# Kernel optimization log

Hardware: AMD Instinct MI355X
Metric: run time of the kernel (lower is better)

Reference implementation:

```python
import jax, jax.numpy as jnp
import numpy as np
import math

B, S, D, H, MAX_LEN = 4, 1024, 1024, 16, 1024
DH = D // H  # 64

def setup_inputs() -> dict:
    key = jax.random.key(0)
    ks = jax.random.split(key, 9)
    s = 1.0 / math.sqrt(D)
    return {
        "q":  jax.random.normal(ks[0], (B, S, D), jnp.float32),
        "kv": jax.random.normal(ks[1], (B, S, D), jnp.float32),
        "Wq": jax.random.normal(ks[2], (D, D), jnp.float32) * s,
        "bq": jax.random.normal(ks[3], (D,), jnp.float32) * s,
        "Wk": jax.random.normal(ks[4], (D, D), jnp.float32) * s,
        "bk": jax.random.normal(ks[5], (D,), jnp.float32) * s,
        "Wv": jax.random.normal(ks[6], (D, D), jnp.float32) * s,
        "bv": jax.random.normal(ks[7], (D,), jnp.float32) * s,
        "Er": jax.random.normal(ks[8], (MAX_LEN, DH), jnp.float32),
    }

def _skew(QEr):
    # QEr: [B, H, S, S]. Music-Transformer skew trick:
    # pad one zero column on the left, reshape, drop first row.
    b, h, r, c = QEr.shape
    padded = jnp.pad(QEr, ((0, 0), (0, 0), (0, 0), (1, 0)))  # [b,h,r,c+1]
    reshaped = padded.reshape(b, h, c + 1, r)
    return reshaped[:, :, 1:, :]  # [b,h,r,c]

def reference(q, kv, Wq, bq, Wk, bk, Wv, bv, Er):
    b, s, d = kv.shape
    # projections (nn.Linear: x @ W + b with W stored [in,out])
    k = (kv @ Wk + bk).reshape(b, s, H, DH).transpose(0, 2, 3, 1)  # [b,h,dh,s]
    v = (kv @ Wv + bv).reshape(b, s, H, DH).transpose(0, 2, 1, 3)  # [b,h,s,dh]
    qh = (q @ Wq + bq).reshape(b, s, H, DH).transpose(0, 2, 1, 3)  # [b,h,s,dh]
    # relative position scores
    Er_t = Er[MAX_LEN - s:, :].T            # [dh, s]
    QEr = jnp.einsum('bhsd,dt->bhst', qh, Er_t)
    Srel = _skew(QEr)                        # [b,h,s,s]
    # content scores
    QK = jnp.einsum('bhsd,bhdt->bhst', qh, k)
    attn = (QK + Srel) / math.sqrt(DH)
    causal = jnp.tril(jnp.ones((s, s), dtype=bool))[None, None]
    attn = jnp.where(causal, attn, -jnp.inf)
    attn = jax.nn.softmax(attn, axis=-1)
    out = jnp.einsum('bhst,bhtd->bhsd', attn, v)
    out = out.transpose(0, 2, 1, 3).reshape(b, s, d)
    return out  # dropout is identity (p=0 / eval)
```

## Files before the change

kernel.cpp:

```cpp
#include <hip/hip_runtime.h>
#include <hip/hip_bf16.h>

typedef __bf16 bf16x8 __attribute__((ext_vector_type(8)));
typedef __bf16 bf16x4 __attribute__((ext_vector_type(4)));
typedef float  f32x4  __attribute__((ext_vector_type(4)));
typedef unsigned __attribute__((may_alias)) u32a;

#define MFMA_B16(a, b, c) __builtin_amdgcn_mfma_f32_16x16x32_bf16((a), (b), (c), 0, 0, 0)

static constexpr int Bk  = 4;
static constexpr int Sk  = 1024;
static constexpr int Dk  = 1024;
static constexpr int Hk  = 16;
static constexpr int DHk = 64;

static constexpr size_t QH_OFF = 0;
static constexpr size_t K_OFF  = 4194304;
static constexpr size_t VT_OFF = 8388608;
static constexpr size_t WT_OFF = 12582912;
static constexpr size_t ER_OFF = 15728640;
static constexpr size_t WS_ELEMS = 15794176;

__device__ __forceinline__ void load_lds16(const void* g, void* l) {
    __builtin_amdgcn_global_load_lds((const __attribute__((address_space(1))) void*)g,
                                     (__attribute__((address_space(3))) void*)l, 16, 0, 0);
}

template<int CTRL>
__device__ __forceinline__ float dppf(float x) {
    int v = __builtin_bit_cast(int, x);
    return __builtin_bit_cast(float,
        __builtin_amdgcn_update_dpp(v, v, CTRL, 0xF, 0xF, false));
}
__device__ __forceinline__ float rmax16(float x) {
    x = fmaxf(x, dppf<0x128>(x));
    x = fmaxf(x, dppf<0x124>(x));
    x = fmaxf(x, dppf<0x122>(x));
    x = fmaxf(x, dppf<0x121>(x));
    return x;
}
__device__ __forceinline__ float rsum16(float x) {
    x += dppf<0x128>(x);
    x += dppf<0x124>(x);
    x += dppf<0x122>(x);
    x += dppf<0x121>(x);
    return x;
}
__device__ __forceinline__ unsigned pk_bf16(float lo, float hi) {
    unsigned r;
    asm("v_cvt_pk_bf16_f32 %0, %1, %2" : "=v"(r) : "v"(lo), "v"(hi));
    return r;
}

__global__ void prep_kernel(const float* __restrict__ Wq, const float* __restrict__ Wk,
                            const float* __restrict__ Wv, const float* __restrict__ Er,
                            __bf16* __restrict__ wt, __bf16* __restrict__ erb)
{
    __shared__ float tile[64][65];
    const int z = blockIdx.z;
    const int tid = threadIdx.x;
    if (z == 3) {
        int idx = (blockIdx.y * 16 + blockIdx.x) * 256 + tid;
        erb[idx] = (__bf16)Er[idx];
        return;
    }
    const float* W = (z == 0) ? Wq : (z == 1 ? Wk : Wv);
    __bf16* dst = wt + (size_t)z * Dk * Dk;
    const int k0 = blockIdx.y * 64, n0 = blockIdx.x * 64;
    #pragma unroll
    for (int j = 0; j < 16; ++j) {
        int idx = tid + j * 256; int r = idx >> 6, c = idx & 63;
        tile[r][c] = W[(size_t)(k0 + r) * Dk + n0 + c];
    }
    __syncthreads();
    #pragma unroll
    for (int j = 0; j < 16; ++j) {
        int idx = tid + j * 256; int r = idx >> 6, c = idx & 63;
        dst[(size_t)(n0 + r) * Dk + k0 + c] = (__bf16)tile[c][r];
    }
}

__global__ __launch_bounds__(256) void proj_kernel(
    const float* __restrict__ Xq, const float* __restrict__ Xkv,
    const float* __restrict__ bq, const float* __restrict__ bk,
    const float* __restrict__ bv, const __bf16* __restrict__ wt,
    __bf16* __restrict__ qh, __bf16* __restrict__ kws, __bf16* __restrict__ vt)
{
    __shared__ __align__(16) float  Al[128 * 32];
    __shared__ __align__(16) __bf16 Bl[128 * 32];

    const int z = blockIdx.z;
    const float* X    = (z == 0) ? Xq : Xkv;
    const float* bias = (z == 0) ? bq : (z == 1 ? bk : bv);
    const __bf16* Wz  = wt + (size_t)z * Dk * Dk;

    const int m0   = blockIdx.x * 128;
    const int n0   = blockIdx.y * 128;
    const int tid  = threadIdx.x;
    const int lane = tid & 63;
    const int w    = tid >> 6;
    const int wr   = w >> 1, wc = w & 1;
    const int l15  = lane & 15;
    const int g    = lane >> 4;

    const float* asrc[4];
    int adst[4];
    #pragma unroll
    for (int i = 0; i < 4; ++i) {
        const int c = w * 4 + i;
        asrc[i] = X + (size_t)(m0 + c * 8 + (lane >> 3)) * Dk + (((lane & 7) ^ (lane >> 3)) << 2);
        adst[i] = c * 1024 + lane * 16;
    }
    const __bf16* bsrc[2];
    int bdst[2];
    #pragma unroll
    for (int i = 0; i < 2; ++i) {
        const int c = w * 2 + i;
        bsrc[i] = Wz + (size_t)(n0 + c * 16 + (lane >> 2)) * Dk + (((lane & 3) ^ ((lane >> 3) & 3)) << 3);
        bdst[i] = c * 1024 + lane * 16;
    }

    int aoff0[4], aoff1[4], boff[4];
    #pragma unroll
    for (int m = 0; m < 4; ++m) {
        const int row = wr * 64 + m * 16 + l15;
        aoff0[m] = row * 128 + (((2 * g)     ^ (l15 & 7)) << 4);
        aoff1[m] = row * 128 + (((2 * g + 1) ^ (l15 & 7)) << 4);
    }
    #pragma unroll
    for (int n = 0; n < 4; ++n) {
        const int row = wc * 64 + n * 16 + l15;
        boff[n] = row * 64 + ((g ^ ((l15 >> 1) & 3)) << 4);
    }

    const f32x4 fz = {0.f, 0.f, 0.f, 0.f};
    f32x4 acc[4][4];
    #pragma unroll
    for (int m = 0; m < 4; ++m)
        #pragma unroll
        for (int n = 0; n < 4; ++n) acc[m][n] = fz;

    const char* Alc = (const char*)Al;
    const char* Blc = (const char*)Bl;

    for (int ks = 0; ks < Dk / 32; ++ks) {
        #pragma unroll
        for (int i = 0; i < 4; ++i)
            load_lds16(asrc[i], (char*)Al + adst[i]);
        #pragma unroll
        for (int i = 0; i < 2; ++i)
            load_lds16(bsrc[i], (char*)Bl + bdst[i]);
        #pragma unroll
        for (int i = 0; i < 4; ++i) asrc[i] += 32;
        #pragma unroll
        for (int i = 0; i < 2; ++i) bsrc[i] += 32;
        __syncthreads();

        bf16x8 bf[4];
        #pragma unroll
        for (int n = 0; n < 4; ++n)
            bf[n] = *(const bf16x8*)(Blc + boff[n]);
        bf16x8 af[4];
        #pragma unroll
        for (int m = 0; m < 4; ++m) {
            f32x4 x0 = *(const f32x4*)(Alc + aoff0[m]);
            f32x4 x1 = *(const f32x4*)(Alc + aoff1[m]);
            bf16x8 a;
            a[0] = (__bf16)x0[0]; a[1] = (__bf16)x0[1]; a[2] = (__bf16)x0[2]; a[3] = (__bf16)x0[3];
            a[4] = (__bf16)x1[0]; a[5] = (__bf16)x1[1]; a[6] = (__bf16)x1[2]; a[7] = (__bf16)x1[3];
            af[m] = a;
        }

        #pragma unroll
        for (int m = 0; m < 4; ++m)
            #pragma unroll
            for (int n = 0; n < 4; ++n)
                acc[m][n] = MFMA_B16(af[m], bf[n], acc[m][n]);
        __syncthreads();
    }

    #pragma unroll
    for (int n = 0; n < 4; ++n) {
        const float bb = bias[n0 + wc * 64 + n * 16 + l15];
        #pragma unroll
        for (int m = 0; m < 4; ++m)
            #pragma unroll
            for (int r = 0; r < 4; ++r) acc[m][n][r] += bb;
    }

    const int b   = m0 >> 10;
    const int s0t = (m0 & 1023) + wr * 64;
    const int h   = (n0 + wc * 64) >> 6;

    if (z < 2) {
        __bf16* dst = (z == 0) ? qh : kws;
        const size_t rowbase = (size_t)(b * Hk + h) * Sk;
        #pragma unroll
        for (int m = 0; m < 4; ++m) {
            #pragma unroll
            for (int r = 0; r < 4; ++r) {
                const int s = s0t + m * 16 + g * 4 + r;
                __bf16* drow = dst + (rowbase + s) * DHk;
                #pragma unroll
                for (int n = 0; n < 4; ++n)
                    drow[n * 16 + l15] = (__bf16)acc[m][n][r];
            }
        }
    } else {
        const size_t hb = (size_t)(b * Hk + h) * DHk;
        #pragma unroll
        for (int m = 0; m < 4; ++m) {
            const int sb = s0t + m * 16 + g * 4;
            #pragma unroll
            for (int n = 0; n < 4; ++n) {
                const int dh = n * 16 + l15;
                bf16x4 pk;
                #pragma unroll
                for (int r = 0; r < 4; ++r) pk[r] = (__bf16)acc[m][n][r];
                *(bf16x4*)(vt + (hb + dh) * Sk + sb) = pk;
            }
        }
    }
}

__device__ __forceinline__ void front_tile(
    const char* Kc, const __bf16* __restrict__ erb, int jb, int l15, int g,
    const bf16x8 (&aq)[2], f32x4 (&sc)[4], f32x4 (&gf)[5])
{
    const f32x4 fz = {0.f, 0.f, 0.f, 0.f};
    #pragma unroll
    for (int j = 0; j < 4; ++j) sc[j] = fz;
    #pragma unroll
    for (int jj = 0; jj < 5; ++jj) gf[jj] = fz;
    #pragma unroll
    for (int kt = 0; kt < 2; ++kt) {
        bf16x8 kb[4];
        #pragma unroll
        for (int j = 0; j < 4; ++j)
            kb[j] = *(const bf16x8*)(Kc + (j * 16 + l15) * 128 + ((((kt << 2) | g) ^ (l15 & 7)) << 4));
        __builtin_amdgcn_s_setprio(1);
        #pragma unroll
        for (int j = 0; j < 4; ++j)
            sc[j] = MFMA_B16(aq[kt], kb[j], sc[j]);
        __builtin_amdgcn_s_setprio(0);
    }
    #pragma unroll
    for (int kt = 0; kt < 2; ++kt) {
        bf16x8 ec[5];
        #pragma unroll
        for (int jj = 0; jj < 5; ++jj) {
            int jr = jb + jj * 16 + l15;
            jr = (jr > 1023) ? 1023 : jr;
            ec[jj] = *(const bf16x8*)(erb + (size_t)jr * DHk + kt * 32 + g * 8);
        }
        __builtin_amdgcn_s_setprio(1);
        #pragma unroll
        for (int jj = 0; jj < 5; ++jj)
            gf[jj] = MFMA_B16(aq[kt], ec[jj], gf[jj]);
        __builtin_amdgcn_s_setprio(0);
    }
}

__global__ __launch_bounds__(256, 3) void attn_kernel(
    const __bf16* __restrict__ qh, const __bf16* __restrict__ kws,
    const __bf16* __restrict__ vt, const __bf16* __restrict__ erb,
    float* __restrict__ out)
{
    __shared__ __align__(16) __bf16 Kl[2][4096];
    __shared__ __align__(16) __bf16 Vl[3][4096];
    __shared__ __align__(16) __bf16 P_lds[4][16][64];

    const int tid  = threadIdx.x;
    const int lane = tid & 63;
    const int w    = tid >> 6;
    const int l15  = lane & 15;
    const int g    = lane >> 4;

    const int lid   = blockIdx.x;
    const int bh    = lid & 63;
    const int strip = 15 - (lid >> 6);
    const int ntw   = strip + 1;
    const int sw    = strip * 64 + w * 16;

    const __bf16* kbase = kws + (size_t)bh * Sk * DHk;
    const __bf16* vbase = vt  + (size_t)bh * DHk * Sk;
    const __bf16* qbase = qh  + ((size_t)bh * Sk + sw) * DHk;

    __bf16 (*Pw)[64] = P_lds[w];

    const int trow   = tid >> 3;
    const int tslot  = tid & 7;
    const int srcoff = (tslot ^ (trow & 7)) << 3;
    char* kd0 = (char*)Kl + tid * 16;
    char* vd0 = (char*)Vl + tid * 16;

    bf16x8 aq[2];
    aq[0] = *(const bf16x8*)(qbase + l15 * DHk + g * 8);
    aq[1] = *(const bf16x8*)(qbase + l15 * DHk + 32 + g * 8);

    const f32x4 fz = {0.f, 0.f, 0.f, 0.f};
    f32x4 O[4];
    float m_[4], l_[4];
    #pragma unroll
    for (int n = 0; n < 4; ++n) O[n] = fz;
    #pragma unroll
    for (int r = 0; r < 4; ++r) { m_[r] = -1e30f; l_[r] = 0.f; }

    const float SCL = 0.125f * 1.44269504088896f;

    load_lds16(kbase + (size_t)trow * DHk + srcoff,        kd0);
    load_lds16(kbase + (size_t)(32 + trow) * DHk + srcoff, kd0 + 4096);
    load_lds16(vbase + (size_t)trow * Sk + srcoff,         vd0);
    load_lds16(vbase + (size_t)(32 + trow) * Sk + srcoff,  vd0 + 4096);
    __builtin_amdgcn_sched_barrier(0);
    asm volatile("s_waitcnt vmcnt(0)" ::: "memory");
    __builtin_amdgcn_sched_barrier(0);
    __builtin_amdgcn_s_barrier();
    __builtin_amdgcn_sched_barrier(0);

    f32x4 scA[4], scB[4], gf[5];
    front_tile((const char*)Kl, erb, 1008 - sw, l15, g, aq, scA, gf);

    int vcur = 0, vnxt = 1;

    for (int it = 0; it < ntw; ++it) {
        const int t0  = it * 64;
        const int cur = it & 1;
        const bool more = (it + 1 < ntw);

        if (more) {
            const int t0n = t0 + 64;
            char* kd = kd0 + (cur ^ 1) * 8192;
            char* vd = (char*)Vl + vnxt * 8192 + tid * 16;
            load_lds16(kbase + (size_t)(t0n + trow) * DHk + srcoff,      kd);
            load_lds16(kbase + (size_t)(t0n + 32 + trow) * DHk + srcoff, kd + 4096);
            load_lds16(vbase + (size_t)trow * Sk + t0n + srcoff,         vd);
            load_lds16(vbase + (size_t)(32 + trow) * Sk + t0n + srcoff,  vd + 4096);
        }
        __builtin_amdgcn_sched_barrier(0);
        asm volatile("s_waitcnt vmcnt(0)" ::: "memory");
        __builtin_amdgcn_sched_barrier(0);
        __builtin_amdgcn_s_barrier();
        __builtin_amdgcn_sched_barrier(0);

        #pragma unroll
        for (int r = 0; r < 4; ++r) {
            const int rr  = g * 4 + r;
            const int sft = 15 - rr;
            const int src = (g << 4) + ((l15 + sft) & 15);
            const bool hi = (l15 + sft) >= 16;
            float h[5];
            #pragma unroll
            for (int jj = 0; jj < 5; ++jj) h[jj] = __shfl(gf[jj][r], src);
            const int s = sw + rr;
            #pragma unroll
            for (int j = 0; j < 4; ++j) {
                float gval = hi ? h[j + 1] : h[j];
                float v = (scA[j][r] + gval) * SCL;
                int t = t0 + j * 16 + l15;
                scA[j][r] = (t > s) ? -1e30f : v;
            }
        }

        if (more)
            front_tile((const char*)Kl + (cur ^ 1) * 8192, erb,
                       t0 + 64 - sw + 1008, l15, g, aq, scB, gf);

        float mt[4];
        #pragma unroll
        for (int r = 0; r < 4; ++r)
            mt[r] = rmax16(fmaxf(fmaxf(scA[0][r], scA[1][r]), fmaxf(scA[2][r], scA[3][r])));

        bool grow = (mt[0] > m_[0] + 8.f) || (mt[1] > m_[1] + 8.f) ||
                    (mt[2] > m_[2] + 8.f) || (mt[3] > m_[3] + 8.f);
        if (__any(grow)) {
            #pragma unroll
            for (int r = 0; r < 4; ++r) {
                float mnew = fmaxf(m_[r], mt[r]);
                float scl  = exp2f(m_[r] - mnew);
                l_[r] *= scl;
                m_[r]  = mnew;
                #pragma unroll
                for (int n = 0; n < 4; ++n) O[n][r] *= scl;
            }
        }
        #pragma unroll
        for (int r = 0; r < 4; ++r) {
            float rs = 0.f;
            #pragma unroll
            for (int j = 0; j < 4; ++j) {
                float p = exp2f(scA[j][r] - m_[r]);
                scA[j][r] = p; rs += p;
            }
            l_[r] += rsum16(rs);
        }

        {
            const int p01 = l15 & 1;
            #pragma unroll
            for (int j = 0; j < 4; ++j) {
                const int slot = 2 * j + (l15 >> 3);
                #pragma unroll
                for (int h2 = 0; h2 < 2; ++h2) {
                    float a0 = scA[j][h2];
                    float a2 = scA[j][h2 + 2];
                    float b0 = dppf<0xB1>(a0);
                    float b2 = dppf<0xB1>(a2);
                    float lo = p01 ? b2 : a0;
                    float hi = p01 ? a2 : b0;
                    unsigned wd = pk_bf16(lo, hi);
                    const int row = g * 4 + h2 + (p01 ? 2 : 0);
                    const int byteoff = row * 128 + (((slot ^ (row & 7)) << 4) | ((l15 & 6) << 1));
                    *(u32a*)((char*)Pw + byteoff) = wd;
                }
            }
        }
        asm volatile("" ::: "memory");
        __builtin_amdgcn_sched_barrier(0);

        const char* Vc = (const char*)Vl + vcur * 8192;
        __builtin_amdgcn_s_setprio(1);
        #pragma unroll
        for (int kt = 0; kt < 2; ++kt) {
            bf16x8 pa = *(const bf16x8*)((const char*)Pw + l15 * 128 +
                                         ((((kt << 2) | g) ^ (l15 & 7)) << 4));
            #pragma unroll
            for (int n = 0; n < 4; ++n) {
                bf16x8 vbf = *(const bf16x8*)(Vc + (n * 16 + l15) * 128 + ((((kt << 2) | g) ^ (l15 & 7)) << 4));
                O[n] = MFMA_B16(pa, vbf, O[n]);
            }
        }
        __builtin_amdgcn_s_setprio(0);

        if (more) {
            #pragma unroll
            for (int j = 0; j < 4; ++j) scA[j] = scB[j];
        }
        vcur = vnxt;
        vnxt = (vnxt == 2) ? 0 : vnxt + 1;
    }

    const int b = bh >> 4, h = bh & 15;
    float* obase = out + ((size_t)b * Sk + sw) * Dk + h * DHk;
    #pragma unroll
    for (int r = 0; r < 4; ++r) {
        float inv = 1.f / l_[r];
        #pragma unroll
        for (int n = 0; n < 4; ++n)
            obase[(size_t)(g * 4 + r) * Dk + n * 16 + l15] = O[n][r] * inv;
    }
}

extern "C" void kernel_launch(void* const* d_in, const int* in_sizes, int n_in,
                              void* d_out, int out_size, void* d_ws, size_t ws_size,
                              hipStream_t stream)
{
    const float* q  = (const float*)d_in[0];
    const float* kv = (const float*)d_in[1];
    const float* Wq = (const float*)d_in[2];
    const float* bq = (const float*)d_in[3];
    const float* Wk = (const float*)d_in[4];
    const float* bk = (const float*)d_in[5];
    const float* Wv = (const float*)d_in[6];
    const float* bv = (const float*)d_in[7];
    const float* Er = (const float*)d_in[8];
    float* out = (float*)d_out;

    if (ws_size < WS_ELEMS * sizeof(__bf16)) return;
    __bf16* ws  = (__bf16*)d_ws;
    __bf16* qh  = ws + QH_OFF;
    __bf16* kws = ws + K_OFF;
    __bf16* vt  = ws + VT_OFF;
    __bf16* wt  = ws + WT_OFF;
    __bf16* erb = ws + ER_OFF;

    prep_kernel<<<dim3(16, 16, 4), 256, 0, stream>>>(Wq, Wk, Wv, Er, wt, erb);
    proj_kernel<<<dim3(32, 8, 3), 256, 0, stream>>>(q, kv, bq, bk, bv, wt, qh, kws, vt);
    attn_kernel<<<dim3(1024), 256, 0, stream>>>(qh, kws, vt, erb, out);
}
```

Baseline: 108.7 us.

## Prefetch K/V tiles two iterations ahead so loads overlap compute

The attention loop used to issue the next K/V tile load and then wait on vmcnt(0) right away, so the global-to-LDS transfer was fully exposed. Now tile 1 is loaded in the prologue, and each iteration issues tile it+2 after the barrier. The loads then run during the whole score, softmax and PV computation. Buffer indexing moves from rotating counters to it&1 for the K double buffer and it%3 for the V triple buffer. The risk is that buffer reuse is now tighter, which is correctness-sensitive, and that there is extra index arithmetic per iteration.

```diff
diff --git a/kernel.cpp b/kernel.cpp
--- a/kernel.cpp
+++ b/kernel.cpp
@@ -318,30 +318,35 @@
     __builtin_amdgcn_s_barrier();
     __builtin_amdgcn_sched_barrier(0);
 
+    if (ntw > 1) {
+        load_lds16(kbase + (size_t)(64 + trow) * DHk + srcoff,      kd0 + 8192);
+        load_lds16(kbase + (size_t)(64 + 32 + trow) * DHk + srcoff, kd0 + 8192 + 4096);
+        load_lds16(vbase + (size_t)trow * Sk + 64 + srcoff,         vd0 + 8192);
+        load_lds16(vbase + (size_t)(32 + trow) * Sk + 64 + srcoff,  vd0 + 8192 + 4096);
+    }
+
     f32x4 scA[4], scB[4], gf[5];
     front_tile((const char*)Kl, erb, 1008 - sw, l15, g, aq, scA, gf);
 
-    int vcur = 0, vnxt = 1;
-
     for (int it = 0; it < ntw; ++it) {
-        const int t0  = it * 64;
-        const int cur = it & 1;
+        const int t0   = it * 64;
         const bool more = (it + 1 < ntw);
 
-        if (more) {
-            const int t0n = t0 + 64;
-            char* kd = kd0 + (cur ^ 1) * 8192;
-            char* vd = (char*)Vl + vnxt * 8192 + tid * 16;
-            load_lds16(kbase + (size_t)(t0n + trow) * DHk + srcoff,      kd);
-            load_lds16(kbase + (size_t)(t0n + 32 + trow) * DHk + srcoff, kd + 4096);
-            load_lds16(vbase + (size_t)trow * Sk + t0n + srcoff,         vd);
-            load_lds16(vbase + (size_t)(32 + trow) * Sk + t0n + srcoff,  vd + 4096);
-        }
         __builtin_amdgcn_sched_barrier(0);
         asm volatile("s_waitcnt vmcnt(0)" ::: "memory");
         __builtin_amdgcn_sched_barrier(0);
         __builtin_amdgcn_s_barrier();
         __builtin_amdgcn_sched_barrier(0);
+
+        if (it + 2 < ntw) {
+            const int t0n2 = t0 + 128;
+            char* kd = kd0 + (it & 1) * 8192;
+            char* vd = (char*)Vl + ((it + 2) % 3) * 8192 + tid * 16;
+            load_lds16(kbase + (size_t)(t0n2 + trow) * DHk + srcoff,      kd);
+            load_lds16(kbase + (size_t)(t0n2 + 32 + trow) * DHk + srcoff, kd + 4096);
+            load_lds16(vbase + (size_t)trow * Sk + t0n2 + srcoff,         vd);
+            load_lds16(vbase + (size_t)(32 + trow) * Sk + t0n2 + srcoff,  vd + 4096);
+        }
 
         #pragma unroll
         for (int r = 0; r < 4; ++r) {
@@ -363,7 +368,7 @@
         }
 
         if (more)
-            front_tile((const char*)Kl + (cur ^ 1) * 8192, erb,
+            front_tile((const char*)Kl + ((it + 1) & 1) * 8192, erb,
                        t0 + 64 - sw + 1008, l15, g, aq, scB, gf);
 
         float mt[4];
@@ -418,7 +423,7 @@
         asm volatile("" ::: "memory");
         __builtin_amdgcn_sched_barrier(0);
 
-        const char* Vc = (const char*)Vl + vcur * 8192;
+        const char* Vc = (const char*)Vl + (it % 3) * 8192;
         __builtin_amdgcn_s_setprio(1);
         #pragma unroll
         for (int kt = 0; kt < 2; ++kt) {
@@ -436,8 +441,6 @@
             #pragma unroll
             for (int j = 0; j < 4; ++j) scA[j] = scB[j];
         }
-        vcur = vnxt;
-        vnxt = (vnxt == 2) ? 0 : vnxt + 1;
     }
 
     const int b = bh >> 4, h = bh & 15;
```

Result: no change. 107.3 us (-1.3%).
